# Kernel optimization log

Hardware: AMD Instinct MI355X
Metric: run time of the kernel (lower is better)

## Reference

```python
import jax, jax.numpy as jnp
import numpy as np

EMBED_DIM = 2048
NUM_HEADS = 16
HEAD_DIM = EMBED_DIM // NUM_HEADS


def setup_inputs() -> dict:
    key = jax.random.key(0)
    ks = jax.random.split(key, 9)
    s = 1.0 / np.sqrt(EMBED_DIM)
    x = jax.random.normal(ks[0], (2, 2048, EMBED_DIM), dtype=jnp.float32)
    Wq = jax.random.uniform(ks[1], (EMBED_DIM, EMBED_DIM), jnp.float32, -s, s)
    bq = jax.random.uniform(ks[2], (EMBED_DIM,), jnp.float32, -s, s)
    Wk = jax.random.uniform(ks[3], (EMBED_DIM, EMBED_DIM), jnp.float32, -s, s)
    bk = jax.random.uniform(ks[4], (EMBED_DIM,), jnp.float32, -s, s)
    Wv = jax.random.uniform(ks[5], (EMBED_DIM, EMBED_DIM), jnp.float32, -s, s)
    bv = jax.random.uniform(ks[6], (EMBED_DIM,), jnp.float32, -s, s)
    Wo = jax.random.uniform(ks[7], (EMBED_DIM, EMBED_DIM), jnp.float32, -s, s)
    bo = jax.random.uniform(ks[8], (EMBED_DIM,), jnp.float32, -s, s)
    return {"x": x, "Wq": Wq, "bq": bq, "Wk": Wk, "bk": bk,
            "Wv": Wv, "bv": bv, "Wo": Wo, "bo": bo}


def reference(x, Wq, bq, Wk, bk, Wv, bv, Wo, bo):
    B, S, E = x.shape
    H, D = NUM_HEADS, HEAD_DIM
    # projections (torch Linear: y = x @ W.T + b)
    def proj(W, b):
        return (x @ W.T + b).reshape(B, S, H, D).transpose(0, 2, 1, 3)  # [B,H,S,D]
    q, k, v = proj(Wq, bq), proj(Wk, bk), proj(Wv, bv)
    scores = jnp.einsum('bhqd,bhkd->bhqk', q, k) / np.sqrt(D).astype(np.float32)
    causal = jnp.triu(jnp.ones((S, S), dtype=bool), k=1)
    scores = jnp.where(causal, jnp.float32(-1e9), scores)
    attn = jax.nn.softmax(scores, axis=-1)
    ctx = jnp.einsum('bhqk,bhkd->bhqd', attn, v)
    ctx = ctx.transpose(0, 2, 1, 3).reshape(B, S, E)
    return ctx @ Wo.T + bo
```

## Files before the change

### kernel.cpp

```cpp
#include <hip/hip_runtime.h>
#include <hip/hip_bf16.h>

typedef __bf16 bf16_t;
typedef bf16_t bf16x8 __attribute__((ext_vector_type(8)));
typedef float f32x4 __attribute__((ext_vector_type(4)));

__device__ __forceinline__ f32x4 mfma16(bf16x8 a, bf16x8 b, f32x4 c) {
    return __builtin_amdgcn_mfma_f32_16x16x32_bf16(a, b, c, 0, 0, 0);
}

__device__ __forceinline__ void load16_to_lds(const void* g, void* l) {
    __builtin_amdgcn_global_load_lds(
        (__attribute__((address_space(1))) unsigned int*)g,
        (__attribute__((address_space(3))) unsigned int*)l, 16, 0, 0);
}

__device__ __forceinline__ bf16x8 cvt8(f32x4 a, f32x4 b) {
    bf16x8 r;
    r[0] = (bf16_t)a[0]; r[1] = (bf16_t)a[1]; r[2] = (bf16_t)a[2]; r[3] = (bf16_t)a[3];
    r[4] = (bf16_t)b[0]; r[5] = (bf16_t)b[1]; r[6] = (bf16_t)b[2]; r[7] = (bf16_t)b[3];
    return r;
}

__global__ __launch_bounds__(256)
void cvt_bf16(const float* __restrict__ in, bf16_t* __restrict__ out) {
    const long i = ((long)blockIdx.x * 256 + threadIdx.x) * 8;
    *(bf16x8*)(out + i) = cvt8(*(const f32x4*)(in + i), *(const f32x4*)(in + i + 4));
}

__global__ __launch_bounds__(256)
void cvt3_bf16(const float* __restrict__ s0, const float* __restrict__ s1,
               const float* __restrict__ s2, bf16_t* __restrict__ o0,
               bf16_t* __restrict__ o1, bf16_t* __restrict__ o2) {
    const int y = blockIdx.y;
    const float* s = (y == 0) ? s0 : (y == 1 ? s1 : s2);
    bf16_t* o      = (y == 0) ? o0 : (y == 1 ? o1 : o2);
    const long i = ((long)blockIdx.x * 256 + threadIdx.x) * 8;
    *(bf16x8*)(o + i) = cvt8(*(const f32x4*)(s + i), *(const f32x4*)(s + i + 4));
}

__global__ __launch_bounds__(256)
void gemm_qkv(const bf16_t* __restrict__ X,
              const bf16_t* __restrict__ W0, const bf16_t* __restrict__ W1, const bf16_t* __restrict__ W2,
              const float* __restrict__ B0, const float* __restrict__ B1, const float* __restrict__ B2,
              bf16_t* __restrict__ O0, bf16_t* __restrict__ O1, bf16_t* __restrict__ O2)
{
    __shared__ __align__(16) bf16_t As[128 * 32];
    __shared__ __align__(16) bf16_t Bs[128 * 32];
    const int z = blockIdx.z;
    const bf16_t* W = (z == 0) ? W0 : (z == 1 ? W1 : W2);
    const float* Bv = (z == 0) ? B0 : (z == 1 ? B1 : B2);
    bf16_t* O       = (z == 0) ? O0 : (z == 1 ? O1 : O2);

    const int tid = threadIdx.x;
    const int w = tid >> 6, l = tid & 63;
    const int lm = l & 15, lq = l >> 4;
    const long arow0 = (long)blockIdx.y * 128;
    const long brow0 = (long)blockIdx.x * 128;
    const int wm = (w >> 1) * 64, wn = (w & 1) * 64;

    f32x4 acc[4][4] = {};

    for (int kt = 0; kt < 2048; kt += 32) {
#pragma unroll
        for (int i = 0; i < 2; ++i) {
            const int c = w * 128 + i * 64 + l;
            const int row = c >> 2, ce = (c & 3) * 8;
            load16_to_lds(X + (arow0 + row) * 2048 + kt + ce, As + (w * 2 + i) * 512);
            load16_to_lds(W + (brow0 + row) * 2048 + kt + ce, Bs + (w * 2 + i) * 512);
        }
        __syncthreads();
        bf16x8 af[4], bfr[4];
#pragma unroll
        for (int i = 0; i < 4; ++i)
            af[i] = *(const bf16x8*)(As + (wm + i * 16 + lm) * 32 + lq * 8);
#pragma unroll
        for (int j = 0; j < 4; ++j)
            bfr[j] = *(const bf16x8*)(Bs + (wn + j * 16 + lm) * 32 + lq * 8);
#pragma unroll
        for (int i = 0; i < 4; ++i)
#pragma unroll
            for (int j = 0; j < 4; ++j)
                acc[i][j] = mfma16(af[i], bfr[j], acc[i][j]);
        __syncthreads();
    }

    const float scale = (z == 0) ? 0.08838834764831845f : 1.0f;
#pragma unroll
    for (int j = 0; j < 4; ++j) {
        const int col = (int)brow0 + wn + j * 16 + lm;
        const float bb = Bv[col];
        const int h = col >> 7, d = col & 127;
#pragma unroll
        for (int i = 0; i < 4; ++i) {
            const int rbase = (int)arow0 + wm + i * 16 + lq * 4;
#pragma unroll
            for (int r = 0; r < 4; ++r) {
                const int row = rbase + r;
                const int b = row >> 11, s = row & 2047;
                const float v = (acc[i][j][r] + bb) * scale;
                long idx;
                if (z == 2) idx = ((long)(b * 16 + h) * 128 + d) * 2048 + s;
                else        idx = ((long)(b * 16 + h) * 2048 + s) * 128 + d;
                O[idx] = (bf16_t)v;
            }
        }
    }
}

__global__ __launch_bounds__(256)
void gemm_out(const bf16_t* __restrict__ A, const bf16_t* __restrict__ W,
              const float* __restrict__ Bv, float* __restrict__ O)
{
    __shared__ __align__(16) bf16_t As[128 * 32];
    __shared__ __align__(16) bf16_t Bs[128 * 32];

    const int tid = threadIdx.x;
    const int w = tid >> 6, l = tid & 63;
    const int lm = l & 15, lq = l >> 4;
    const long arow0 = (long)blockIdx.y * 128;
    const long brow0 = (long)blockIdx.x * 128;
    const int wm = (w >> 1) * 64, wn = (w & 1) * 64;

    f32x4 acc[4][4] = {};

    for (int kt = 0; kt < 2048; kt += 32) {
#pragma unroll
        for (int i = 0; i < 2; ++i) {
            const int c = w * 128 + i * 64 + l;
            const int row = c >> 2, ce = (c & 3) * 8;
            load16_to_lds(A + (arow0 + row) * 2048 + kt + ce, As + (w * 2 + i) * 512);
            load16_to_lds(W + (brow0 + row) * 2048 + kt + ce, Bs + (w * 2 + i) * 512);
        }
        __syncthreads();
        bf16x8 af[4], bfr[4];
#pragma unroll
        for (int i = 0; i < 4; ++i)
            af[i] = *(const bf16x8*)(As + (wm + i * 16 + lm) * 32 + lq * 8);
#pragma unroll
        for (int j = 0; j < 4; ++j)
            bfr[j] = *(const bf16x8*)(Bs + (wn + j * 16 + lm) * 32 + lq * 8);
#pragma unroll
        for (int i = 0; i < 4; ++i)
#pragma unroll
            for (int j = 0; j < 4; ++j)
                acc[i][j] = mfma16(af[i], bfr[j], acc[i][j]);
        __syncthreads();
    }

#pragma unroll
    for (int j = 0; j < 4; ++j) {
        const int col = (int)brow0 + wn + j * 16 + lm;
        const float bb = Bv[col];
#pragma unroll
        for (int i = 0; i < 4; ++i) {
            const int rbase = (int)arow0 + wm + i * 16 + lq * 4;
#pragma unroll
            for (int r = 0; r < 4; ++r)
                O[(long)(rbase + r) * 2048 + col] = acc[i][j][r] + bb;
        }
    }
}

__global__ __launch_bounds__(256)
void attn(const bf16_t* __restrict__ Q, const bf16_t* __restrict__ K,
          const bf16_t* __restrict__ VT, bf16_t* __restrict__ CTX)
{
    __shared__ __align__(16) bf16_t Ks[64 * 136];
    __shared__ __align__(16) bf16_t Vs[128 * 72];
    __shared__ __align__(16) bf16_t Ps[4][32 * 72];

    const int tid = threadIdx.x;
    const int w = tid >> 6, l = tid & 63;
    const int lm = l & 15, lq = l >> 4;

    const int flat = blockIdx.x;
    const int half = flat >> 8, idx = flat & 255;
    int qx = idx & 15;
    const int bh = (idx >> 4) + half * 16;
    if (half) qx = 15 - qx;

    const int q0 = qx * 128;
    const int qw = q0 + w * 32;
    const long base = (long)bh * 2048 * 128;

    bf16x8 qf[2][4];
#pragma unroll
    for (int qi = 0; qi < 2; ++qi)
#pragma unroll
        for (int ks = 0; ks < 4; ++ks)
            qf[qi][ks] = *(const bf16x8*)(Q + base + (long)(qw + qi * 16 + lm) * 128 + ks * 32 + lq * 8);

    f32x4 ctx[2][8] = {};
    float mrow[2][4], lrow[2][4];
#pragma unroll
    for (int qi = 0; qi < 2; ++qi)
#pragma unroll
        for (int r = 0; r < 4; ++r) { mrow[qi][r] = -1e30f; lrow[qi][r] = 0.f; }

    const int ntiles = (q0 + 128) >> 6;
    for (int it = 0; it < ntiles; ++it) {
        const int s0 = it << 6;
        bf16x8 rk[4], rv[4];
#pragma unroll
        for (int i = 0; i < 4; ++i) {
            const int c = tid + i * 256;
            const int kk = c >> 4, ock = c & 15;
            rk[i] = *(const bf16x8*)(K + base + (long)(s0 + kk) * 128 + ock * 8);
            const int d = c >> 3, ocv = c & 7;
            rv[i] = *(const bf16x8*)(VT + base + (long)d * 2048 + s0 + ocv * 8);
        }
        __syncthreads();
#pragma unroll
        for (int i = 0; i < 4; ++i) {
            const int c = tid + i * 256;
            const int kk = c >> 4, ock = c & 15;
            *(bf16x8*)(Ks + kk * 136 + ock * 8) = rk[i];
            const int d = c >> 3, ocv = c & 7;
            *(bf16x8*)(Vs + d * 72 + ocv * 8) = rv[i];
        }
        __syncthreads();

        f32x4 sc[2][4] = {};
#pragma unroll
        for (int ks = 0; ks < 4; ++ks)
#pragma unroll
            for (int kj = 0; kj < 4; ++kj) {
                const int kk = kj * 16 + lm;
                const int dc = ks * 4 + lq;
                const bf16x8 kf = *(const bf16x8*)(Ks + kk * 136 + dc * 8);
                sc[0][kj] = mfma16(qf[0][ks], kf, sc[0][kj]);
                sc[1][kj] = mfma16(qf[1][ks], kf, sc[1][kj]);
            }
        if (s0 + 63 > qw) {
#pragma unroll
            for (int qi = 0; qi < 2; ++qi)
#pragma unroll
                for (int kj = 0; kj < 4; ++kj) {
                    const int colg = s0 + kj * 16 + lm;
#pragma unroll
                    for (int r = 0; r < 4; ++r) {
                        const int rowg = qw + qi * 16 + lq * 4 + r;
                        if (colg > rowg) sc[qi][kj][r] = -1e30f;
                    }
                }
        }
#pragma unroll
        for (int qi = 0; qi < 2; ++qi)
#pragma unroll
            for (int r = 0; r < 4; ++r) {
                float mx = fmaxf(fmaxf(sc[qi][0][r], sc[qi][1][r]),
                                 fmaxf(sc[qi][2][r], sc[qi][3][r]));
#pragma unroll
                for (int off = 1; off < 16; off <<= 1)
                    mx = fmaxf(mx, __shfl_xor(mx, off, 64));
                const float mn = fmaxf(mrow[qi][r], mx);
                const float alpha = exp2f((mrow[qi][r] - mn) * 1.4426950408889634f);
                mrow[qi][r] = mn;
                float sum = 0.f;
#pragma unroll
                for (int kj = 0; kj < 4; ++kj) {
                    const float p = exp2f((sc[qi][kj][r] - mn) * 1.4426950408889634f);
                    sc[qi][kj][r] = p;
                    sum += p;
                }
#pragma unroll
                for (int off = 1; off < 16; off <<= 1)
                    sum += __shfl_xor(sum, off, 64);
                lrow[qi][r] = lrow[qi][r] * alpha + sum;
#pragma unroll
                for (int dj = 0; dj < 8; ++dj)
                    ctx[qi][dj][r] *= alpha;
            }
#pragma unroll
        for (int qi = 0; qi < 2; ++qi)
#pragma unroll
            for (int kj = 0; kj < 4; ++kj)
#pragma unroll
                for (int r = 0; r < 4; ++r)
                    Ps[w][(qi * 16 + lq * 4 + r) * 72 + kj * 16 + lm] = (bf16_t)sc[qi][kj][r];
        __syncthreads();
#pragma unroll
        for (int ks2 = 0; ks2 < 2; ++ks2) {
            bf16x8 pf[2];
#pragma unroll
            for (int qi = 0; qi < 2; ++qi)
                pf[qi] = *(const bf16x8*)(&Ps[w][0] + (qi * 16 + lm) * 72 + ks2 * 32 + lq * 8);
#pragma unroll
            for (int dj = 0; dj < 8; ++dj) {
                const int d = dj * 16 + lm;
                const int c8 = ks2 * 4 + lq;
                const bf16x8 vf = *(const bf16x8*)(Vs + d * 72 + c8 * 8);
                ctx[0][dj] = mfma16(pf[0], vf, ctx[0][dj]);
                ctx[1][dj] = mfma16(pf[1], vf, ctx[1][dj]);
            }
        }
    }

    const int b = bh >> 4, h = bh & 15;
#pragma unroll
    for (int qi = 0; qi < 2; ++qi)
#pragma unroll
        for (int r = 0; r < 4; ++r) {
            const float inv = 1.0f / lrow[qi][r];
            const int s = qw + qi * 16 + lq * 4 + r;
#pragma unroll
            for (int dj = 0; dj < 8; ++dj) {
                const int e = h * 128 + dj * 16 + lm;
                CTX[((long)(b * 2048 + s)) * 2048 + e] = (bf16_t)(ctx[qi][dj][r] * inv);
            }
        }
}

extern "C" void kernel_launch(void* const* d_in, const int* in_sizes, int n_in,
                              void* d_out, int out_size, void* d_ws, size_t ws_size,
                              hipStream_t stream)
{
    const float* x  = (const float*)d_in[0];
    const float* Wq = (const float*)d_in[1];
    const float* bq = (const float*)d_in[2];
    const float* Wk = (const float*)d_in[3];
    const float* bk = (const float*)d_in[4];
    const float* Wv = (const float*)d_in[5];
    const float* bv = (const float*)d_in[6];
    const float* Wo = (const float*)d_in[7];
    const float* bo = (const float*)d_in[8];
    float* out = (float*)d_out;

    const size_t NTOK = (size_t)2 * 2048 * 2048;
    const size_t NW   = (size_t)2048 * 2048;
    bf16_t* q  = (bf16_t*)d_ws;
    bf16_t* k  = q  + NTOK;
    bf16_t* vT = k  + NTOK;
    bf16_t* cx = vT + NTOK;
    bf16_t* xb  = cx;
    bf16_t* wob = q;
    bf16_t* wqb = (bf16_t*)d_out;
    bf16_t* wkb = wqb + NW;
    bf16_t* wvb = wkb + NW;

    dim3 blk(256);
    cvt_bf16<<<dim3(4096), blk, 0, stream>>>(x, xb);
    cvt3_bf16<<<dim3(2048, 3), blk, 0, stream>>>(Wq, Wk, Wv, wqb, wkb, wvb);
    gemm_qkv<<<dim3(16, 32, 3), blk, 0, stream>>>(xb, wqb, wkb, wvb, bq, bk, bv, q, k, vT);
    attn<<<dim3(512), blk, 0, stream>>>(q, k, vT, cx);
    cvt_bf16<<<dim3(2048), blk, 0, stream>>>(Wo, wob);
    gemm_out<<<dim3(16, 32), blk, 0, stream>>>(cx, wob, bo, out);
}
```

Before: 515.8 us.

## Halve attention query tile, use direct-to-LDS swizzled loads, merge conversion kernels

The attention kernel now handles 64 query rows per block (16 per wave) rather than 128. The grid doubles to 1024 blocks with a four-way causal load-balancing order, and launch bounds request 4 blocks per CU. K/V tiles are loaded with global_load_lds straight into XOR-swizzled unpadded LDS, and P is written to LDS with the same swizzle, removing the register staging and padding. The x and Wq/Wk/Wv conversions are merged into one launch. The risk is that smaller query tiles reload K/V twice as often per query, trading more memory traffic for better occupancy and CU utilisation.

```diff
diff --git a/kernel.cpp b/kernel.cpp
--- a/kernel.cpp
+++ b/kernel.cpp
@@ -29,12 +29,18 @@
 }
 
 __global__ __launch_bounds__(256)
-void cvt3_bf16(const float* __restrict__ s0, const float* __restrict__ s1,
-               const float* __restrict__ s2, bf16_t* __restrict__ o0,
-               bf16_t* __restrict__ o1, bf16_t* __restrict__ o2) {
+void cvt_all(const float* __restrict__ x,
+             const float* __restrict__ Wq, const float* __restrict__ Wk, const float* __restrict__ Wv,
+             bf16_t* __restrict__ xb, bf16_t* __restrict__ wqb,
+             bf16_t* __restrict__ wkb, bf16_t* __restrict__ wvb) {
+    const long NW = 4194304;
     const int y = blockIdx.y;
-    const float* s = (y == 0) ? s0 : (y == 1 ? s1 : s2);
-    bf16_t* o      = (y == 0) ? o0 : (y == 1 ? o1 : o2);
+    const float* s; bf16_t* o;
+    if      (y == 0) { s = x;      o = xb;      }
+    else if (y == 1) { s = x + NW; o = xb + NW; }
+    else if (y == 2) { s = Wq;     o = wqb;     }
+    else if (y == 3) { s = Wk;     o = wkb;     }
+    else             { s = Wv;     o = wvb;     }
     const long i = ((long)blockIdx.x * 256 + threadIdx.x) * 8;
     *(bf16x8*)(o + i) = cvt8(*(const f32x4*)(s + i), *(const f32x4*)(s + i + 4));
 }
@@ -162,154 +168,131 @@
     }
 }
 
-__global__ __launch_bounds__(256)
+__global__ __launch_bounds__(256, 4)
 void attn(const bf16_t* __restrict__ Q, const bf16_t* __restrict__ K,
           const bf16_t* __restrict__ VT, bf16_t* __restrict__ CTX)
 {
-    __shared__ __align__(16) bf16_t Ks[64 * 136];
-    __shared__ __align__(16) bf16_t Vs[128 * 72];
-    __shared__ __align__(16) bf16_t Ps[4][32 * 72];
+    __shared__ __align__(16) bf16_t Ks[64 * 128];
+    __shared__ __align__(16) bf16_t Vs[128 * 64];
+    __shared__ __align__(16) bf16_t Ps[4][16 * 64];
 
     const int tid = threadIdx.x;
     const int w = tid >> 6, l = tid & 63;
     const int lm = l & 15, lq = l >> 4;
 
     const int flat = blockIdx.x;
-    const int half = flat >> 8, idx = flat & 255;
-    int qx = idx & 15;
-    const int bh = (idx >> 4) + half * 16;
-    if (half) qx = 15 - qx;
-
-    const int q0 = qx * 128;
-    const int qw = q0 + w * 32;
+    const int g = flat >> 8, i0 = flat & 255;
+    const int bh = i0 >> 3, j = i0 & 7;
+    const int qx = (g == 0) ? j : (g == 1) ? (15 - j) : (g == 2) ? (16 + j) : (31 - j);
+
+    const int q0 = qx * 64;
+    const int qw = q0 + w * 16;
     const long base = (long)bh * 2048 * 128;
 
-    bf16x8 qf[2][4];
-#pragma unroll
-    for (int qi = 0; qi < 2; ++qi)
-#pragma unroll
-        for (int ks = 0; ks < 4; ++ks)
-            qf[qi][ks] = *(const bf16x8*)(Q + base + (long)(qw + qi * 16 + lm) * 128 + ks * 32 + lq * 8);
-
-    f32x4 ctx[2][8] = {};
-    float mrow[2][4], lrow[2][4];
-#pragma unroll
-    for (int qi = 0; qi < 2; ++qi)
-#pragma unroll
-        for (int r = 0; r < 4; ++r) { mrow[qi][r] = -1e30f; lrow[qi][r] = 0.f; }
-
-    const int ntiles = (q0 + 128) >> 6;
+    bf16x8 qf[4];
+#pragma unroll
+    for (int ks = 0; ks < 4; ++ks)
+        qf[ks] = *(const bf16x8*)(Q + base + (long)(qw + lm) * 128 + ks * 32 + lq * 8);
+
+    f32x4 ctx[8] = {};
+    float mrow[4], lrow[4];
+#pragma unroll
+    for (int r = 0; r < 4; ++r) { mrow[r] = -1e30f; lrow[r] = 0.f; }
+
+    const int ntiles = qx + 1;
     for (int it = 0; it < ntiles; ++it) {
         const int s0 = it << 6;
-        bf16x8 rk[4], rv[4];
+        __syncthreads();
 #pragma unroll
         for (int i = 0; i < 4; ++i) {
-            const int c = tid + i * 256;
-            const int kk = c >> 4, ock = c & 15;
-            rk[i] = *(const bf16x8*)(K + base + (long)(s0 + kk) * 128 + ock * 8);
-            const int d = c >> 3, ocv = c & 7;
-            rv[i] = *(const bf16x8*)(VT + base + (long)d * 2048 + s0 + ocv * 8);
-        }
-        __syncthreads();
-#pragma unroll
-        for (int i = 0; i < 4; ++i) {
-            const int c = tid + i * 256;
-            const int kk = c >> 4, ock = c & 15;
-            *(bf16x8*)(Ks + kk * 136 + ock * 8) = rk[i];
-            const int d = c >> 3, ocv = c & 7;
-            *(bf16x8*)(Vs + d * 72 + ocv * 8) = rv[i];
-        }
-        __syncthreads();
-
-        f32x4 sc[2][4] = {};
+            const int s = (w * 4 + i) * 64 + l;
+            const int kk = s >> 4, dcs = s & 15;
+            const int dc = dcs ^ (kk & 15);
+            load16_to_lds(K + base + (long)(s0 + kk) * 128 + dc * 8, Ks + (w * 4 + i) * 512);
+            const int d = s >> 3, cs = s & 7;
+            const int c = cs ^ (d & 7);
+            load16_to_lds(VT + base + (long)d * 2048 + s0 + c * 8, Vs + (w * 4 + i) * 512);
+        }
+        __syncthreads();
+
+        f32x4 sc[4] = {};
 #pragma unroll
         for (int ks = 0; ks < 4; ++ks)
 #pragma unroll
             for (int kj = 0; kj < 4; ++kj) {
                 const int kk = kj * 16 + lm;
                 const int dc = ks * 4 + lq;
-                const bf16x8 kf = *(const bf16x8*)(Ks + kk * 136 + dc * 8);
-                sc[0][kj] = mfma16(qf[0][ks], kf, sc[0][kj]);
-                sc[1][kj] = mfma16(qf[1][ks], kf, sc[1][kj]);
+                const bf16x8 kf = *(const bf16x8*)(Ks + (kk * 16 + (dc ^ (kk & 15))) * 8);
+                sc[kj] = mfma16(qf[ks], kf, sc[kj]);
             }
         if (s0 + 63 > qw) {
 #pragma unroll
-            for (int qi = 0; qi < 2; ++qi)
-#pragma unroll
-                for (int kj = 0; kj < 4; ++kj) {
-                    const int colg = s0 + kj * 16 + lm;
-#pragma unroll
-                    for (int r = 0; r < 4; ++r) {
-                        const int rowg = qw + qi * 16 + lq * 4 + r;
-                        if (colg > rowg) sc[qi][kj][r] = -1e30f;
-                    }
+            for (int kj = 0; kj < 4; ++kj) {
+                const int colg = s0 + kj * 16 + lm;
+#pragma unroll
+                for (int r = 0; r < 4; ++r) {
+                    const int rowg = qw + lq * 4 + r;
+                    if (colg > rowg) sc[kj][r] = -1e30f;
                 }
-        }
-#pragma unroll
-        for (int qi = 0; qi < 2; ++qi)
+            }
+        }
+#pragma unroll
+        for (int r = 0; r < 4; ++r) {
+            float mx = fmaxf(fmaxf(sc[0][r], sc[1][r]), fmaxf(sc[2][r], sc[3][r]));
+#pragma unroll
+            for (int off = 1; off < 16; off <<= 1)
+                mx = fmaxf(mx, __shfl_xor(mx, off, 64));
+            const float mn = fmaxf(mrow[r], mx);
+            const float alpha = exp2f((mrow[r] - mn) * 1.4426950408889634f);
+            mrow[r] = mn;
+            float sum = 0.f;
+#pragma unroll
+            for (int kj = 0; kj < 4; ++kj) {
+                const float p = exp2f((sc[kj][r] - mn) * 1.4426950408889634f);
+                sc[kj][r] = p;
+                sum += p;
+            }
+#pragma unroll
+            for (int off = 1; off < 16; off <<= 1)
+                sum += __shfl_xor(sum, off, 64);
+            lrow[r] = lrow[r] * alpha + sum;
+#pragma unroll
+            for (int dj = 0; dj < 8; ++dj)
+                ctx[dj][r] *= alpha;
+        }
+#pragma unroll
+        for (int kj = 0; kj < 4; ++kj)
 #pragma unroll
             for (int r = 0; r < 4; ++r) {
-                float mx = fmaxf(fmaxf(sc[qi][0][r], sc[qi][1][r]),
-                                 fmaxf(sc[qi][2][r], sc[qi][3][r]));
-#pragma unroll
-                for (int off = 1; off < 16; off <<= 1)
-                    mx = fmaxf(mx, __shfl_xor(mx, off, 64));
-                const float mn = fmaxf(mrow[qi][r], mx);
-                const float alpha = exp2f((mrow[qi][r] - mn) * 1.4426950408889634f);
-                mrow[qi][r] = mn;
-                float sum = 0.f;
-#pragma unroll
-                for (int kj = 0; kj < 4; ++kj) {
-                    const float p = exp2f((sc[qi][kj][r] - mn) * 1.4426950408889634f);
-                    sc[qi][kj][r] = p;
-                    sum += p;
-                }
-#pragma unroll
-                for (int off = 1; off < 16; off <<= 1)
-                    sum += __shfl_xor(sum, off, 64);
-                lrow[qi][r] = lrow[qi][r] * alpha + sum;
-#pragma unroll
-                for (int dj = 0; dj < 8; ++dj)
-                    ctx[qi][dj][r] *= alpha;
-            }
-#pragma unroll
-        for (int qi = 0; qi < 2; ++qi)
-#pragma unroll
-            for (int kj = 0; kj < 4; ++kj)
-#pragma unroll
-                for (int r = 0; r < 4; ++r)
-                    Ps[w][(qi * 16 + lq * 4 + r) * 72 + kj * 16 + lm] = (bf16_t)sc[qi][kj][r];
+                const int q = lq * 4 + r;
+                const int kk = kj * 16 + lm;
+                Ps[w][q * 64 + ((kk >> 3) ^ (q & 7)) * 8 + (kk & 7)] = (bf16_t)sc[kj][r];
+            }
         __syncthreads();
 #pragma unroll
         for (int ks2 = 0; ks2 < 2; ++ks2) {
-            bf16x8 pf[2];
-#pragma unroll
-            for (int qi = 0; qi < 2; ++qi)
-                pf[qi] = *(const bf16x8*)(&Ps[w][0] + (qi * 16 + lm) * 72 + ks2 * 32 + lq * 8);
+            const int c = ks2 * 4 + lq;
+            const bf16x8 pf = *(const bf16x8*)(&Ps[w][0] + lm * 64 + (c ^ (lm & 7)) * 8);
 #pragma unroll
             for (int dj = 0; dj < 8; ++dj) {
                 const int d = dj * 16 + lm;
-                const int c8 = ks2 * 4 + lq;
-                const bf16x8 vf = *(const bf16x8*)(Vs + d * 72 + c8 * 8);
-                ctx[0][dj] = mfma16(pf[0], vf, ctx[0][dj]);
-                ctx[1][dj] = mfma16(pf[1], vf, ctx[1][dj]);
+                const bf16x8 vf = *(const bf16x8*)(Vs + (d * 8 + (c ^ (d & 7))) * 8);
+                ctx[dj] = mfma16(pf, vf, ctx[dj]);
             }
         }
     }
 
     const int b = bh >> 4, h = bh & 15;
 #pragma unroll
-    for (int qi = 0; qi < 2; ++qi)
-#pragma unroll
-        for (int r = 0; r < 4; ++r) {
-            const float inv = 1.0f / lrow[qi][r];
-            const int s = qw + qi * 16 + lq * 4 + r;
-#pragma unroll
-            for (int dj = 0; dj < 8; ++dj) {
-                const int e = h * 128 + dj * 16 + lm;
-                CTX[((long)(b * 2048 + s)) * 2048 + e] = (bf16_t)(ctx[qi][dj][r] * inv);
-            }
-        }
+    for (int r = 0; r < 4; ++r) {
+        const float inv = 1.0f / lrow[r];
+        const int s = qw + lq * 4 + r;
+#pragma unroll
+        for (int dj = 0; dj < 8; ++dj) {
+            const int e = h * 128 + dj * 16 + lm;
+            CTX[((long)(b * 2048 + s)) * 2048 + e] = (bf16_t)(ctx[dj][r] * inv);
+        }
+    }
 }
 
 extern "C" void kernel_launch(void* const* d_in, const int* in_sizes, int n_in,
@@ -340,10 +323,9 @@
     bf16_t* wvb = wkb + NW;
 
     dim3 blk(256);
-    cvt_bf16<<<dim3(4096), blk, 0, stream>>>(x, xb);
-    cvt3_bf16<<<dim3(2048, 3), blk, 0, stream>>>(Wq, Wk, Wv, wqb, wkb, wvb);
+    cvt_all<<<dim3(2048, 5), blk, 0, stream>>>(x, Wq, Wk, Wv, xb, wqb, wkb, wvb);
     gemm_qkv<<<dim3(16, 32, 3), blk, 0, stream>>>(xb, wqb, wkb, wvb, bq, bk, bv, q, k, vT);
-    attn<<<dim3(512), blk, 0, stream>>>(q, k, vT, cx);
+    attn<<<dim3(1024), blk, 0, stream>>>(q, k, vT, cx);
     cvt_bf16<<<dim3(2048), blk, 0, stream>>>(Wo, wob);
     gemm_out<<<dim3(16, 32), blk, 0, stream>>>(cx, wob, bo, out);
 }
```

Result: faster. 496.6 us (-3.7%).
